# Optimization experiments

Hardware: AMD Instinct MI355X
Metric: run time of the kernel (lower is better)

## Reference

```python
import jax, jax.numpy as jnp
import numpy as np

B, T, D, H = 128, 512, 256, 256


def setup_inputs() -> dict:
    key = jax.random.key(0)
    k1, k2, k3, k4 = jax.random.split(key, 4)
    x = jax.random.normal(k1, (B, T, D), dtype=jnp.float32)
    x_len = jax.random.randint(k2, (B,), 1, T + 1)  # lengths in [1, T]
    W_ih = jax.random.normal(k3, (4 * H, D), dtype=jnp.float32) * 0.05
    W_hh = jax.random.normal(k4, (4 * H, H), dtype=jnp.float32) * 0.05
    b_ih = jnp.zeros((4 * H,), dtype=jnp.float32)
    # reset_params: bias_hh forget-gate chunk (index 1 of i,f,g,o) set to 1
    b_hh = jnp.zeros((4 * H,), dtype=jnp.float32).at[H:2 * H].set(1.0)
    return {"x": x, "x_len": x_len, "W_ih": W_ih, "W_hh": W_hh,
            "b_ih": b_ih, "b_hh": b_hh}


def reference(x, x_len, W_ih, W_hh, b_ih, b_hh):
    # Dropout is identity in eval mode. The sort/pack/unpack pipeline is
    # mathematically equivalent to running a masked LSTM over the padded
    # batch and zeroing outputs at positions t >= x_len (pad_packed_sequence
    # zero-pads), since output at t < len only depends on steps <= t.
    Bx, Tx, _ = x.shape
    Hh = W_hh.shape[1]
    # Precompute input projections for all timesteps: [B, T, 4H] -> [T, B, 4H]
    xg = jnp.einsum('btd,gd->btg', x, W_ih) + b_ih + b_hh
    xg = jnp.swapaxes(xg, 0, 1)

    def step(carry, xt):
        h, c = carry
        gates = xt + h @ W_hh.T  # [B, 4H]
        i, f, g, o = jnp.split(gates, 4, axis=-1)
        i = jax.nn.sigmoid(i)
        f = jax.nn.sigmoid(f)
        g = jnp.tanh(g)
        o = jax.nn.sigmoid(o)
        c = f * c + i * g
        h = o * jnp.tanh(c)
        return (h, c), h

    h0 = jnp.zeros((Bx, Hh), x.dtype)
    (_, _), hs = jax.lax.scan(step, (h0, h0), xg)  # hs: [T, B, H]
    out = jnp.swapaxes(hs, 0, 1)  # [B, T, H]
    mask = jnp.arange(Tx)[None, :] < x_len[:, None]  # [B, T]
    return jnp.where(mask[..., None], out, jnp.zeros((), x.dtype))
```

## Files before the change

### kernel.cpp

```cpp
#include <hip/hip_runtime.h>
#include <hip/hip_fp16.h>
#include <math.h>

#define BB 128
#define TT 512
#define DD 256
#define HH 256
#define NG 1024

typedef _Float16 h2_t __attribute__((ext_vector_type(2)));
typedef _Float16 f16x8 __attribute__((ext_vector_type(8)));
typedef float f32x4 __attribute__((ext_vector_type(4)));

#if __has_builtin(__builtin_amdgcn_fdot2)
__device__ __forceinline__ float fdot2_(h2_t a, h2_t b, float c) {
    return __builtin_amdgcn_fdot2(a, b, c, false);
}
#else
__device__ __forceinline__ float fdot2_(h2_t a, h2_t b, float c) {
    return c + (float)a.x * (float)b.x + (float)a.y * (float)b.y;
}
#endif

__device__ __forceinline__ float sigmoidf_(float x) {
    return 1.0f / (1.0f + __expf(-x));
}
__device__ __forceinline__ float tanhf_(float x) {
    x = fminf(15.0f, fmaxf(-15.0f, x));
    float e = __expf(2.0f * x);
    return (e - 1.0f) / (e + 1.0f);
}
__device__ __forceinline__ void dot4_(float4& acc, uint4 u, h2_t h) {
    acc.x = fdot2_(__builtin_bit_cast(h2_t, u.x), h, acc.x);
    acc.y = fdot2_(__builtin_bit_cast(h2_t, u.y), h, acc.y);
    acc.z = fdot2_(__builtin_bit_cast(h2_t, u.z), h, acc.z);
    acc.w = fdot2_(__builtin_bit_cast(h2_t, u.w), h, acc.w);
}

#if __has_builtin(__builtin_amdgcn_update_dpp)
__device__ __forceinline__ float pair_sum_(float v) {
    int x = __builtin_bit_cast(int, v);
    int y = __builtin_amdgcn_update_dpp(0, x, 0xB1, 0xF, 0xF, true);
    return v + __builtin_bit_cast(float, y);
}
#else
__device__ __forceinline__ float pair_sum_(float v) {
    return v + __shfl_xor(v, 1, 64);
}
#endif

__global__ void pack2(const float* __restrict__ W_ih, const float* __restrict__ W_hh,
                      const float* __restrict__ b_ih, const float* __restrict__ b_hh,
                      __half* __restrict__ Wg16, __half* __restrict__ Wi16,
                      __half* __restrict__ Wh16, float* __restrict__ bias_p) {
    int idx = blockIdx.x * 256 + threadIdx.x;
    int n = idx >> 8;
    int k = idx & 255;
    int g = (n & 3) * 256 + (n >> 2);
    float wih = W_ih[g * 256 + k];
    float whh = W_hh[g * 256 + k];
    Wg16[n * 256 + k] = __float2half(wih);
    size_t hidx = ((size_t)(k >> 1) * 1024 + n) * 2 + (k & 1);
    Wi16[hidx] = __float2half(wih);
    Wh16[hidx] = __float2half(whh);
    if (idx < 1024) {
        int gg = (idx & 3) * 256 + (idx >> 2);
        bias_p[idx] = b_ih[gg] + b_hh[gg];
    }
}

__global__ __launch_bounds__(256) void cvt_x(const float* __restrict__ X,
                                             __half* __restrict__ X16) {
    size_t i = ((size_t)blockIdx.x * 256 + threadIdx.x) * 8;
    float4 a = *(const float4*)&X[i];
    float4 b = *(const float4*)&X[i + 4];
    f16x8 v;
    v[0] = (_Float16)a.x; v[1] = (_Float16)a.y; v[2] = (_Float16)a.z; v[3] = (_Float16)a.w;
    v[4] = (_Float16)b.x; v[5] = (_Float16)b.y; v[6] = (_Float16)b.z; v[7] = (_Float16)b.w;
    *(f16x8*)&X16[i] = v;
}

__global__ __launch_bounds__(256) void xg_gemm_mfma(const __half* __restrict__ X16,
                                                    const __half* __restrict__ Wg16,
                                                    const float* __restrict__ bias_p,
                                                    __half* __restrict__ xg,
                                                    int t0, int lTc, int tcMask) {
    __shared__ __align__(16) __half st[4][16][72];
    int tid = threadIdx.x;
    int w = tid >> 6, lane = tid & 63;
    int row16 = lane & 15, quad = lane >> 4;
    int m0 = blockIdx.x * 64 + w * 16;

    int mrow = m0 + row16;
    size_t xrow = (size_t)(mrow >> lTc) * 512 + t0 + (mrow & tcMask);
    const __half* aptr = X16 + xrow * 256 + quad * 8;
    f16x8 afrag[8];
#pragma unroll
    for (int kk = 0; kk < 8; ++kk)
        afrag[kk] = *(const f16x8*)(aptr + kk * 32);

    int ml = lane >> 2, cq = lane & 3;
    int mout = blockIdx.x * 64 + w * 16 + ml;
    __half* xgo = xg + (size_t)mout * 1024 + cq * 16;

    for (int n0 = 0; n0 < 1024; n0 += 64) {
#pragma unroll
        for (int cg = 0; cg < 4; ++cg) {
            int n = n0 + cg * 16 + row16;
            const __half* bptr = Wg16 + (size_t)n * 256 + quad * 8;
            f32x4 acc = {0.0f, 0.0f, 0.0f, 0.0f};
#pragma unroll
            for (int kk = 0; kk < 8; ++kk) {
                f16x8 bfrag = *(const f16x8*)(bptr + kk * 32);
                acc = __builtin_amdgcn_mfma_f32_16x16x32_f16(afrag[kk], bfrag, acc, 0, 0, 0);
            }
            float bias = bias_p[n];
#pragma unroll
            for (int r = 0; r < 4; ++r)
                st[w][quad * 4 + r][cg * 16 + row16] = __float2half(acc[r] + bias);
        }
        __syncthreads();
        const uint4* src = (const uint4*)&st[w][ml][cq * 16];
        uint4 v0 = src[0], v1 = src[1];
        *(uint4*)&xgo[n0] = v0;
        *(uint4*)&xgo[n0 + 8] = v1;
        __syncthreads();
    }
}

__global__ __launch_bounds__(512, 2) void lstm_rec4(const __half* __restrict__ xg,
                                                    const __half* __restrict__ Wh16,
                                                    const int* __restrict__ x_len,
                                                    float* __restrict__ out,
                                                    __half* __restrict__ h_state,
                                                    float* __restrict__ c_state,
                                                    int t0, int Tc) {
    __shared__ __align__(16) uint4 lw[9728];
    __shared__ __align__(16) __half hs[2][272];
    int tid = threadIdx.x;
    int c = tid >> 1, kh = tid & 1;
    int b = blockIdx.x;
    int len = x_len[b];
    const uint4* W4 = (const uint4*)Wh16;

    for (int j = tid; j < 9728; j += 512) {
        int i2 = j >> 9, c2 = (j >> 1) & 255, kh2 = j & 1;
        lw[j] = W4[(size_t)(kh2 * 64 + 44 + i2) * 256 + c2];
    }
    const uint4* wp = W4 + (size_t)(kh * 64) * 256 + c;
    uint4 wreg[44];
#pragma unroll
    for (int i = 0; i < 44; ++i) wreg[i] = wp[(size_t)i * 256];

    float cst = 0.0f;
    float hlast = 0.0f;
    if (t0 != 0) cst = c_state[b * 256 + c];
    if (kh == 0)
        hs[0][c + ((c >> 7) << 4)] = (t0 == 0) ? __float2half(0.0f)
                                               : h_state[b * 256 + c];

    const __half* xgb = xg + (size_t)b * Tc * 1024 + 4 * c;
    float* outb = out + ((size_t)b * 512 + t0) * 256 + c;
    const uint4* lwb = lw + tid;
    __syncthreads();

    for (int tt = 0; tt < Tc; ++tt) {
        uint4 s0 = wp[(size_t)63 * 256];
        uint2 xr = *(const uint2*)(xgb + (size_t)tt * 1024);

        const uint4* h4 = (const uint4*)(hs[tt & 1]) + kh * 18;
        float4 acc = {0.0f, 0.0f, 0.0f, 0.0f};
#pragma unroll
        for (int j = 0; j < 11; ++j) {
            uint4 hv = h4[j];
            dot4_(acc, wreg[j * 4 + 0], __builtin_bit_cast(h2_t, hv.x));
            dot4_(acc, wreg[j * 4 + 1], __builtin_bit_cast(h2_t, hv.y));
            dot4_(acc, wreg[j * 4 + 2], __builtin_bit_cast(h2_t, hv.z));
            dot4_(acc, wreg[j * 4 + 3], __builtin_bit_cast(h2_t, hv.w));
        }
#pragma unroll
        for (int j = 11; j < 15; ++j) {
            uint4 hv = h4[j];
            int i0 = (j - 11) * 4;
            dot4_(acc, lwb[(i0 + 0) * 512], __builtin_bit_cast(h2_t, hv.x));
            dot4_(acc, lwb[(i0 + 1) * 512], __builtin_bit_cast(h2_t, hv.y));
            dot4_(acc, lwb[(i0 + 2) * 512], __builtin_bit_cast(h2_t, hv.z));
            dot4_(acc, lwb[(i0 + 3) * 512], __builtin_bit_cast(h2_t, hv.w));
        }
        {
            uint4 hv = h4[15];
            dot4_(acc, lwb[16 * 512], __builtin_bit_cast(h2_t, hv.x));
            dot4_(acc, lwb[17 * 512], __builtin_bit_cast(h2_t, hv.y));
            dot4_(acc, lwb[18 * 512], __builtin_bit_cast(h2_t, hv.z));
            dot4_(acc, s0, __builtin_bit_cast(h2_t, hv.w));
        }
        float gi = pair_sum_(acc.x);
        float gf = pair_sum_(acc.y);
        float gg = pair_sum_(acc.z);
        float go = pair_sum_(acc.w);
        h2_t x01 = __builtin_bit_cast(h2_t, xr.x);
        h2_t x23 = __builtin_bit_cast(h2_t, xr.y);
        gi += (float)x01.x;
        gf += (float)x01.y;
        gg += (float)x23.x;
        go += (float)x23.y;
        float iv = sigmoidf_(gi), fv = sigmoidf_(gf);
        float gv = tanhf_(gg),   ov = sigmoidf_(go);
        cst = fv * cst + iv * gv;
        float h = ov * tanhf_(cst);
        hlast = h;
        if (kh == 0) {
            outb[(size_t)tt * 256] = (t0 + tt < len) ? h : 0.0f;
            hs[(tt & 1) ^ 1][c + ((c >> 7) << 4)] = __float2half(h);
        }
        __syncthreads();
    }
    if (kh == 0) {
        h_state[b * 256 + c] = __float2half(hlast);
        c_state[b * 256 + c] = cst;
    }
}

__global__ __launch_bounds__(1024) void lstm_fused16(const float* __restrict__ X,
                                                     const __half* __restrict__ Wi16,
                                                     const __half* __restrict__ Wh16,
                                                     const float* __restrict__ bias_p,
                                                     const int* __restrict__ x_len,
                                                     float* __restrict__ out) {
    __shared__ __half hs_h[256];
    __shared__ __half xs_h[256];
    __shared__ float4 part[3][256];
    int tid = threadIdx.x;
    int c = tid & 255, kh = tid >> 8;
    int b = blockIdx.x;
    int len = x_len[b];
    float cst = 0.0f;
    float4 bias;
    if (kh == 0) {
        bias = *(const float4*)&bias_p[4 * c];
        hs_h[c] = __float2half(0.0f);
    }
    const uint4* wph = (const uint4*)(Wh16 + (size_t)(kh * 32) * 2048 + 8 * c);
    const uint4* wpi = (const uint4*)(Wi16 + (size_t)(kh * 32) * 2048 + 8 * c);
    float* outb = out + (size_t)b * 512 * 256 + c;
    __syncthreads();

    for (int t = 0; t < TT; ++t) {
        if (tid < 128) {
            float2 xv = *(const float2*)&X[((size_t)b * 512 + t) * 256 + 2 * tid];
            h2_t xh = {(_Float16)xv.x, (_Float16)xv.y};
            ((h2_t*)xs_h)[tid] = xh;
        }
        __syncthreads();
        float4 acc = {0.0f, 0.0f, 0.0f, 0.0f};
#pragma unroll 4
        for (int i = 0; i < 32; ++i) {
            uint4 uh = wph[(size_t)i * 256];
            uint4 ui = wpi[(size_t)i * 256];
            h2_t hv = ((const h2_t*)hs_h)[kh * 32 + i];
            h2_t xv = ((const h2_t*)xs_h)[kh * 32 + i];
            dot4_(acc, uh, hv);
            dot4_(acc, ui, xv);
        }
        if (kh) part[kh - 1][c] = acc;
        __syncthreads();
        if (kh == 0) {
            float4 p0 = part[0][c], p1 = part[1][c], p2 = part[2][c];
            float gi = acc.x + p0.x + p1.x + p2.x + bias.x;
            float gf = acc.y + p0.y + p1.y + p2.y + bias.y;
            float gg = acc.z + p0.z + p1.z + p2.z + bias.z;
            float go = acc.w + p0.w + p1.w + p2.w + bias.w;
            float iv = sigmoidf_(gi), fv = sigmoidf_(gf);
            float gv = tanhf_(gg),   ov = sigmoidf_(go);
            cst = fv * cst + iv * gv;
            float h = ov * tanhf_(cst);
            outb[(size_t)t * 256] = (t < len) ? h : 0.0f;
            hs_h[c] = __float2half(h);
        }
        __syncthreads();
    }
}

extern "C" void kernel_launch(void* const* d_in, const int* in_sizes, int n_in,
                              void* d_out, int out_size, void* d_ws, size_t ws_size,
                              hipStream_t stream) {
    const float* x     = (const float*)d_in[0];
    const int*   x_len = (const int*)d_in[1];
    const float* W_ih  = (const float*)d_in[2];
    const float* W_hh  = (const float*)d_in[3];
    const float* b_ih  = (const float*)d_in[4];
    const float* b_hh  = (const float*)d_in[5];
    float* out = (float*)d_out;

    char* ws = (char*)d_ws;
    __half* Wh16    = (__half*)(ws);
    __half* Wi16    = (__half*)(ws + 0x080000);
    __half* Wg16    = (__half*)(ws + 0x100000);
    float*  bias_p  = (float*)(ws + 0x180000);
    __half* h_state = (__half*)(ws + 0x181000);
    float*  c_state = (float*)(ws + 0x191000);
    __half* x16     = (__half*)(ws + 0x1B1000);
    size_t  o_xg    = 0x1B1000 + (size_t)0x2004000;
    __half* xg      = (__half*)(ws + o_xg);

    int Tc = 0;
    for (int cand = 512; cand >= 16; cand >>= 1)
        if (ws_size >= o_xg + (size_t)cand * 262144) { Tc = cand; break; }

    pack2<<<1024, 256, 0, stream>>>(W_ih, W_hh, b_ih, b_hh,
                                    Wg16, Wi16, Wh16, bias_p);
    if (Tc) {
        cvt_x<<<8192, 256, 0, stream>>>(x, x16);
        int lTc = 31 - __builtin_clz((unsigned)Tc);
        for (int t0 = 0; t0 < TT; t0 += Tc) {
            xg_gemm_mfma<<<2 * Tc, 256, 0, stream>>>(x16, Wg16, bias_p, xg,
                                                     t0, lTc, Tc - 1);
            lstm_rec4<<<BB, 512, 0, stream>>>(xg, Wh16, x_len, out,
                                              h_state, c_state, t0, Tc);
        }
    } else {
        lstm_fused16<<<BB, 1024, 0, stream>>>(x, Wi16, Wh16, bias_p, x_len, out);
    }
}
```

Baseline: 1.194 ms.

## Fuse x fp16 conversion into GEMM and stage weight tiles in LDS

Removes the separate cvt_x kernel and instead converts fp32 inputs to fp16 while loading the A fragments inside the input-projection GEMM. Weight tiles are now staged through a swizzled shared-memory buffer with register prefetch of the next 64-column tile, so global B reads are not repeated per wave. Dropping the x16 buffer also frees workspace, which may allow a larger time chunk Tc. The cost is extra LDS use and register pressure in the GEMM kernel.

```diff
diff --git a/kernel.cpp b/kernel.cpp
--- a/kernel.cpp
+++ b/kernel.cpp
@@ -69,22 +69,12 @@
     }
 }
 
-__global__ __launch_bounds__(256) void cvt_x(const float* __restrict__ X,
-                                             __half* __restrict__ X16) {
-    size_t i = ((size_t)blockIdx.x * 256 + threadIdx.x) * 8;
-    float4 a = *(const float4*)&X[i];
-    float4 b = *(const float4*)&X[i + 4];
-    f16x8 v;
-    v[0] = (_Float16)a.x; v[1] = (_Float16)a.y; v[2] = (_Float16)a.z; v[3] = (_Float16)a.w;
-    v[4] = (_Float16)b.x; v[5] = (_Float16)b.y; v[6] = (_Float16)b.z; v[7] = (_Float16)b.w;
-    *(f16x8*)&X16[i] = v;
-}
-
-__global__ __launch_bounds__(256) void xg_gemm_mfma(const __half* __restrict__ X16,
+__global__ __launch_bounds__(256) void xg_gemm_mfma(const float* __restrict__ X,
                                                     const __half* __restrict__ Wg16,
                                                     const float* __restrict__ bias_p,
                                                     __half* __restrict__ xg,
                                                     int t0, int lTc, int tcMask) {
+    __shared__ __align__(16) uint4 bs[2048];
     __shared__ __align__(16) __half st[4][16][72];
     int tid = threadIdx.x;
     int w = tid >> 6, lane = tid & 63;
@@ -93,37 +83,75 @@
 
     int mrow = m0 + row16;
     size_t xrow = (size_t)(mrow >> lTc) * 512 + t0 + (mrow & tcMask);
-    const __half* aptr = X16 + xrow * 256 + quad * 8;
+    const float* aptr = X + xrow * 256 + quad * 8;
     f16x8 afrag[8];
 #pragma unroll
-    for (int kk = 0; kk < 8; ++kk)
-        afrag[kk] = *(const f16x8*)(aptr + kk * 32);
+    for (int kk = 0; kk < 8; ++kk) {
+        float4 a = *(const float4*)(aptr + kk * 32);
+        float4 b = *(const float4*)(aptr + kk * 32 + 4);
+        f16x8 v;
+        v[0] = (_Float16)a.x; v[1] = (_Float16)a.y; v[2] = (_Float16)a.z; v[3] = (_Float16)a.w;
+        v[4] = (_Float16)b.x; v[5] = (_Float16)b.y; v[6] = (_Float16)b.z; v[7] = (_Float16)b.w;
+        afrag[kk] = v;
+    }
+
+    const uint4* Bg = (const uint4*)Wg16;
+    uint4 breg[8];
+#pragma unroll
+    for (int i = 0; i < 8; ++i) {
+        int idx = tid + i * 256;
+        int r = idx >> 5, u = idx & 31;
+        breg[i] = Bg[(size_t)r * 32 + u];
+    }
+#pragma unroll
+    for (int i = 0; i < 8; ++i) {
+        int idx = tid + i * 256;
+        int r = idx >> 5, u = idx & 31;
+        bs[r * 32 + ((u + r) & 31)] = breg[i];
+    }
+    __syncthreads();
 
     int ml = lane >> 2, cq = lane & 3;
     int mout = blockIdx.x * 64 + w * 16 + ml;
     __half* xgo = xg + (size_t)mout * 1024 + cq * 16;
 
     for (int n0 = 0; n0 < 1024; n0 += 64) {
+        if (n0 + 64 < 1024) {
+#pragma unroll
+            for (int i = 0; i < 8; ++i) {
+                int idx = tid + i * 256;
+                int r = idx >> 5, u = idx & 31;
+                breg[i] = Bg[(size_t)(n0 + 64 + r) * 32 + u];
+            }
+        }
 #pragma unroll
         for (int cg = 0; cg < 4; ++cg) {
-            int n = n0 + cg * 16 + row16;
-            const __half* bptr = Wg16 + (size_t)n * 256 + quad * 8;
+            int r = cg * 16 + row16;
             f32x4 acc = {0.0f, 0.0f, 0.0f, 0.0f};
 #pragma unroll
             for (int kk = 0; kk < 8; ++kk) {
-                f16x8 bfrag = *(const f16x8*)(bptr + kk * 32);
+                int u = quad + 4 * kk;
+                f16x8 bfrag = __builtin_bit_cast(f16x8, bs[r * 32 + ((u + r) & 31)]);
                 acc = __builtin_amdgcn_mfma_f32_16x16x32_f16(afrag[kk], bfrag, acc, 0, 0, 0);
             }
-            float bias = bias_p[n];
-#pragma unroll
-            for (int r = 0; r < 4; ++r)
-                st[w][quad * 4 + r][cg * 16 + row16] = __float2half(acc[r] + bias);
+            float bias = bias_p[n0 + cg * 16 + row16];
+#pragma unroll
+            for (int q = 0; q < 4; ++q)
+                st[w][quad * 4 + q][cg * 16 + row16] = __float2half(acc[q] + bias);
         }
         __syncthreads();
         const uint4* src = (const uint4*)&st[w][ml][cq * 16];
         uint4 v0 = src[0], v1 = src[1];
         *(uint4*)&xgo[n0] = v0;
         *(uint4*)&xgo[n0 + 8] = v1;
+        if (n0 + 64 < 1024) {
+#pragma unroll
+            for (int i = 0; i < 8; ++i) {
+                int idx = tid + i * 256;
+                int r = idx >> 5, u = idx & 31;
+                bs[r * 32 + ((u + r) & 31)] = breg[i];
+            }
+        }
         __syncthreads();
     }
 }
@@ -299,21 +327,18 @@
     float*  bias_p  = (float*)(ws + 0x180000);
     __half* h_state = (__half*)(ws + 0x181000);
     float*  c_state = (float*)(ws + 0x191000);
-    __half* x16     = (__half*)(ws + 0x1B1000);
-    size_t  o_xg    = 0x1B1000 + (size_t)0x2004000;
-    __half* xg      = (__half*)(ws + o_xg);
+    __half* xg      = (__half*)(ws + 0x1B1000);
 
     int Tc = 0;
     for (int cand = 512; cand >= 16; cand >>= 1)
-        if (ws_size >= o_xg + (size_t)cand * 262144) { Tc = cand; break; }
+        if (ws_size >= 0x1B1000 + (size_t)cand * 262144) { Tc = cand; break; }
 
     pack2<<<1024, 256, 0, stream>>>(W_ih, W_hh, b_ih, b_hh,
                                     Wg16, Wi16, Wh16, bias_p);
     if (Tc) {
-        cvt_x<<<8192, 256, 0, stream>>>(x, x16);
         int lTc = 31 - __builtin_clz((unsigned)Tc);
         for (int t0 = 0; t0 < TT; t0 += Tc) {
-            xg_gemm_mfma<<<2 * Tc, 256, 0, stream>>>(x16, Wg16, bias_p, xg,
+            xg_gemm_mfma<<<2 * Tc, 256, 0, stream>>>(x, Wg16, bias_p, xg,
                                                      t0, lTc, Tc - 1);
             lstm_rec4<<<BB, 512, 0, stream>>>(xg, Wh16, x_len, out,
                                               h_state, c_state, t0, Tc);
```

Result: faster. 1.105 ms (-7.4%).
